# Kernel tuning notes

Hardware: AMD Instinct MI355X
Metric: run time of the kernel (lower is better)

## Reference

```python
import jax, jax.numpy as jnp
import numpy as np

B, C, H, W = 2, 256, 120, 240
HID = 512  # mlp_ratio=2 * embed_dim
EPS = 1e-5


def setup_inputs() -> dict:
    key = jax.random.key(0)
    ks = jax.random.split(key, 10)
    f = lambda k, shp, s=1.0: jax.random.normal(k, shp, jnp.float32) * s
    return {
        'x': f(ks[0], (B, C, H, W)),
        'gamma': f(ks[1], (C,), 0.1),
        'beta': f(ks[2], (C,), 0.1),
        'norm0_w': jnp.ones((C,), jnp.float32),
        'norm0_b': jnp.zeros((C,), jnp.float32),
        'norm1_w': jnp.ones((C,), jnp.float32),
        'norm1_b': jnp.zeros((C,), jnp.float32),
        'w_spec_r': f(ks[3], (C, C), 0.02),
        'w_spec_i': f(ks[4], (C, C), 0.02),
        'inner_w': f(ks[5], (C, C), 0.02),
        'inner_b': jnp.zeros((C,), jnp.float32),
        'mlp_w1': f(ks[6], (HID, C), 0.02),
        'mlp_b1': jnp.zeros((HID,), jnp.float32),
        'mlp_w2': f(ks[7], (C, HID), 0.02),
        'mlp_b2': jnp.zeros((C,), jnp.float32),
    }


def _inorm(x, w, b):
    # InstanceNorm2d (affine): normalize over spatial dims per (batch, channel)
    m = x.mean(axis=(2, 3), keepdims=True)
    v = x.var(axis=(2, 3), keepdims=True)
    xh = (x - m) * jax.lax.rsqrt(v + EPS)
    return xh * w[None, :, None, None] + b[None, :, None, None]


def _conv1x1(x, w, b=None):
    y = jnp.einsum('bihw,oi->bohw', x, w)
    return y if b is None else y + b[None, :, None, None]


def reference(x, gamma, beta, norm0_w, norm0_b, norm1_w, norm1_b,
              w_spec_r, w_spec_i, inner_w, inner_b,
              mlp_w1, mlp_b1, mlp_w2, mlp_b2):
    residual = x
    h = _inorm(x, norm0_w, norm0_b)
    # SpectralConv2d: rfft2 -> channel-mixing complex matmul (all modes kept,
    # hard_thresholding_fraction=1.0) -> irfft2. sparsity_threshold=0 -> no shrink.
    xf = jnp.fft.rfft2(h, norm='ortho')                     # [B,C,H,W//2+1] complex
    wc = (w_spec_r + 1j * w_spec_i).astype(xf.dtype)
    yf = jnp.einsum('bihw,io->bohw', xf, wc)
    h = jnp.fft.irfft2(yf, s=(H, W), norm='ortho')
    # inner skip (1x1 conv of residual) + GELU (linear filter branch)
    h = h + _conv1x1(residual, inner_w, inner_b)
    h = jax.nn.gelu(h, approximate=False)
    h = _inorm(h, norm1_w, norm1_b)
    # FiLM with scale=1
    h = (1.0 + gamma[None, :, None, None]) * h + beta[None, :, None, None]
    # distributed MLP: 1x1 conv -> GELU -> 1x1 conv
    h = _conv1x1(h, mlp_w1, mlp_b1)
    h = jax.nn.gelu(h, approximate=False)
    h = _conv1x1(h, mlp_w2, mlp_b2)
    # outer skip = identity
    return h + residual
```

## Files before the change

### kernel.cpp

```cpp
#include <hip/hip_runtime.h>
#include <hip/hip_bf16.h>

typedef __hip_bfloat16 bf16;
typedef short short8 __attribute__((ext_vector_type(8)));
typedef float f32x4 __attribute__((ext_vector_type(4)));

#define NB 2
#define NC 256
#define NH 120
#define NW 240
#define NHW (NH*NW)
#define NSP 16384
#define NHID 512
#define NPT 450
#define REPS 1e-5f
#define SC_W 0.06454972243679028f
#define SC_H 0.09128709291752769f
#define PI2 6.283185307179586f

__device__ __forceinline__ float gelu_f(float x){ return 0.5f*x*(1.f+erff(x*0.7071067811865476f)); }
__device__ __forceinline__ float us2f(ushort u){ union{float f; uint v;} c; c.v=((uint)u)<<16; return c.f; }
__device__ __forceinline__ ushort f2us(float f){ bf16 b=__float2bfloat16(f); return *(ushort*)&b; }

#define OFF_A0   0
#define OFF_D0   512
#define OFF_A1c  1024
#define OFF_D1c  1536
#define OFF_TWF  2048
#define OFF_THF  34816
#define OFF_THI  67584
#define OFF_TWI  100352
#define OFF_WRT  133120
#define OFF_WIT  165888
#define OFF_IWB  198656
#define OFF_W2B  231424
#define OFF_W1P  296960
#define OFF_B1P  428032
#define OFF_PS   429056
#define OFF_RA   889856
#define OFF_RB   9278464
#define WS_FLOATS 17667072ULL

#define RA0 OFF_RA
#define RA1 (OFF_RA+4194304)
#define RB0 OFF_RB
#define RB1 (OFF_RB+4194304)
#define OFF_FRE RB0
#define OFF_FIM (RB0+3932160)

__global__ __launch_bounds__(256) void k_setup(float* ws, const float* wsr, const float* wsi,
                                               const float* iw, const float* w2){
  int t = blockIdx.x*256 + threadIdx.x;
  if (t < 65536){
    int n=t>>8, w=t&255; float v=0.f;
    if(w<NW){
      if(n<121){ v = cosf(PI2*(float)((n*w)%NW)/(float)NW)*SC_W; }
      else if(n>=128 && n<249){ int k=n-128; v = -sinf(PI2*(float)((k*w)%NW)/(float)NW)*SC_W; }
    }
    ((ushort*)(ws+OFF_TWF))[t]=f2us(v); return;
  } t-=65536;
  if (t < 65536){
    int n=t>>8, j=t&255; float v=0.f;
    int h = j&127; bool im = (j>=128);
    if(h<NH){
      if(n<128){ int m=n; if(m<NH){ float sn,cs; sincosf(PI2*(float)((m*h)%NH)/(float)NH,&sn,&cs);
        v = (im? sn : cs)*SC_H; } }
      else { int m=n-128; if(m<NH){ float sn,cs; sincosf(PI2*(float)((m*h)%NH)/(float)NH,&sn,&cs);
        v = (im? cs : -sn)*SC_H; } }
    }
    ((ushort*)(ws+OFF_THF))[t]=f2us(v); return;
  } t-=65536;
  if (t < 65536){
    int n=t>>8, j=t&255; float v=0.f;
    int m = j&127; bool im = (j>=128);
    if(m<NH){
      if(n<128){ int h=n; if(h<NH){ float sn,cs; sincosf(PI2*(float)((h*m)%NH)/(float)NH,&sn,&cs);
        v = (im? -sn : cs)*SC_H; } }
      else { int h=n-128; if(h<NH){ float sn,cs; sincosf(PI2*(float)((h*m)%NH)/(float)NH,&sn,&cs);
        v = (im? cs : sn)*SC_H; } }
    }
    ((ushort*)(ws+OFF_THI))[t]=f2us(v); return;
  } t-=65536;
  if (t < 65536){
    int w=t>>8, j=t&255; float v=0.f;
    if(w<NW){
      int k = j&127; bool im = (j>=128);
      if(k<121){
        float ck = (k==0||k==120)? 1.f : 2.f;
        float sn,cs; sincosf(PI2*(float)((w*k)%NW)/(float)NW,&sn,&cs);
        v = ck*(im? -sn : cs)*SC_W;
      }
    }
    ((ushort*)(ws+OFF_TWI))[t]=f2us(v); return;
  } t-=65536;
  if (t < 65536){ int o=t>>8,i=t&255; ((ushort*)(ws+OFF_WRT))[t]=f2us(wsr[i*NC+o]); return; } t-=65536;
  if (t < 65536){ int o=t>>8,i=t&255; ((ushort*)(ws+OFF_WIT))[t]=f2us(wsi[i*NC+o]); return; } t-=65536;
  if (t < 65536){ ((ushort*)(ws+OFF_IWB))[t]=f2us(iw[t]); return; } t-=65536;
  if (t < 131072){ ((ushort*)(ws+OFF_W2B))[t]=f2us(w2[t]); return; }
}

__global__ __launch_bounds__(256) void k_stats0(const float* x, const float* n0w, const float* n0b, float* ws){
  int g = blockIdx.x, c = g & (NC-1);
  const float4* xp = (const float4*)(x + (size_t)g*NHW);
  float s=0.f, q=0.f;
  for(int i=threadIdx.x;i<NHW/4;i+=256){
    float4 v=xp[i];
    s+=v.x+v.y+v.z+v.w;
    q=fmaf(v.x,v.x,fmaf(v.y,v.y,fmaf(v.z,v.z,fmaf(v.w,v.w,q))));
  }
  __shared__ float ls[4], lq[4];
  #pragma unroll
  for(int o=32;o>0;o>>=1){ s+=__shfl_down(s,o,64); q+=__shfl_down(q,o,64); }
  int lane=threadIdx.x&63, wid=threadIdx.x>>6;
  if(!lane){ ls[wid]=s; lq[wid]=q; }
  __syncthreads();
  if(!threadIdx.x){
    s=ls[0]+ls[1]+ls[2]+ls[3]; q=lq[0]+lq[1]+lq[2]+lq[3];
    float m=s*(1.f/NHW), var=q*(1.f/NHW)-m*m;
    float r=rsqrtf(var+REPS);
    float a=r*n0w[c];
    ws[OFF_A0+g]=a; ws[OFF_D0+g]=fmaf(-m,a,n0b[c]);
  }
}

__global__ __launch_bounds__(256) void k_norm(const float* x, float* ws){
  int h = blockIdx.x, g = blockIdx.y, t = threadIdx.x;
  float a = ws[OFF_A0+g], d = ws[OFF_D0+g];
  ushort v = 0;
  if(t < NW) v = f2us(fmaf(a, x[(size_t)g*NHW + (size_t)h*NW + t], d));
  ((ushort*)(ws+RA0))[(size_t)g*30720 + (size_t)h*256 + t] = v;
}

template<int SPLIT, int EPI>
__global__ __launch_bounds__(256) void k_sgemm(const ushort* Ap0, const ushort* Ap1, const ushort* Bm,
                                               ushort* O0, ushort* O1, ushort* Ub){
  int nb = blockIdx.x*64, mb = blockIdx.y*256;
  int tid = threadIdx.x, w = tid>>6, l = tid&63, lq = l>>4, lr = l&15;
  const ushort* ar0[4]; const ushort* ar1[4]; const ushort* br[4];
  #pragma unroll
  for(int mt=0;mt<4;mt++){
    size_t r = mb + w*64 + mt*16 + lr;
    ar0[mt] = Ap0 + r*(SPLIT?128:256) + lq*8;
    ar1[mt] = SPLIT ? (Ap1 + r*128 + lq*8) : ar0[mt];
  }
  #pragma unroll
  for(int nt=0;nt<4;nt++) br[nt] = Bm + (size_t)(nb + nt*16 + lr)*256 + lq*8;
  f32x4 acc[4][4] = {};
  #pragma unroll
  for(int kk=0;kk<8;kk++){
    int k = kk*32;
    short8 af[4], bfr[4];
    #pragma unroll
    for(int mt=0;mt<4;mt++){
      const ushort* p = SPLIT ? ((k<128 ? ar0[mt] : ar1[mt]) + (k&127)) : (ar0[mt] + k);
      af[mt] = *(const short8*)p;
    }
    #pragma unroll
    for(int nt=0;nt<4;nt++) bfr[nt] = *(const short8*)(br[nt]+k);
    #pragma unroll
    for(int mt=0;mt<4;mt++)
      #pragma unroll
      for(int nt=0;nt<4;nt++)
        acc[mt][nt] = __builtin_amdgcn_mfma_f32_16x16x32_bf16(af[mt], bfr[nt], acc[mt][nt], 0,0,0);
  }
  #pragma unroll
  for(int mt=0;mt<4;mt++){
    #pragma unroll
    for(int r=0;r<4;r++){
      int m = mb + w*64 + mt*16 + lq*4 + r;
      #pragma unroll
      for(int nt=0;nt<4;nt++){
        int n = nb + nt*16 + lr;
        float v = acc[mt][nt][r];
        if (EPI==0){
          if(n<128) O0[(size_t)m*128+n] = f2us(v);
          else      O1[(size_t)m*128+n-128] = f2us(v);
        } else {
          int g = m>>7, h = m&127;
          if(h<NH && n<NW) Ub[(size_t)g*NHW + (size_t)h*NW + n] = f2us(v);
        }
      }
    }
  }
}

__global__ __launch_bounds__(256) void k_t64(const ushort* src, ushort* dst, int srows, int sgstr){
  __shared__ ushort lt[64][72];
  int g=blockIdx.z, i0=blockIdx.y*64, p0=blockIdx.x*64;
  int t=threadIdx.x, r=t>>2, q=t&3;
  int row = i0 + r;
  uint4 u0=make_uint4(0,0,0,0), u1=u0;
  if(row < srows){
    const ushort* sp = src + (size_t)g*sgstr + (size_t)row*128 + p0 + q*16;
    u0=*(const uint4*)sp; u1=*(const uint4*)(sp+8);
  }
  *(uint4*)&lt[r][q*16]=u0; *(uint4*)&lt[r][q*16+8]=u1;
  __syncthreads();
  int pr=t>>2, q2=t&3;
  union { ushort s[8]; uint4 u; } o0, o1;
  #pragma unroll
  for(int e=0;e<8;e++){ o0.s[e]=lt[q2*16+e][pr]; o1.s[e]=lt[q2*16+8+e][pr]; }
  ushort* dp = dst + (size_t)g*NSP + (size_t)(p0+pr)*128 + i0 + q2*16;
  *(uint4*)dp = o0.u; *(uint4*)(dp+8) = o1.u;
}

__global__ __launch_bounds__(256) void k_tP(const ushort* src, ushort* dst){
  __shared__ ushort lt[64][72];
  int b=blockIdx.z, i0=blockIdx.y*64, p0=blockIdx.x*64;
  int t=threadIdx.x, r=t>>2, q=t&3;
  const ushort* sp = src + (size_t)(b*NC+i0+r)*NSP + p0 + q*16;
  uint4 u0=*(const uint4*)sp, u1=*(const uint4*)(sp+8);
  *(uint4*)&lt[r][q*16]=u0; *(uint4*)&lt[r][q*16+8]=u1;
  __syncthreads();
  int pr=t>>2, q2=t&3;
  union { ushort s[8]; uint4 u; } o0, o1;
  #pragma unroll
  for(int e=0;e<8;e++){ o0.s[e]=lt[q2*16+e][pr]; o1.s[e]=lt[q2*16+8+e][pr]; }
  ushort* dp = dst + ((size_t)b*NSP + p0 + pr)*NC + i0 + q2*16;
  *(uint4*)dp = o0.u; *(uint4*)(dp+8) = o1.u;
}

__global__ __launch_bounds__(256) void k_mixg(float* ws){
  int b = blockIdx.z, p0 = blockIdx.x*32;
  int tid = threadIdx.x, w = tid>>6, l = tid&63, lq = l>>4, lr = l&15;
  const ushort* Wr = (const ushort*)(ws+OFF_WRT);
  const ushort* Wi = (const ushort*)(ws+OFF_WIT);
  const ushort* Gr = (const ushort*)(ws+RA0) + (size_t)b*NSP*NC;
  const ushort* Gi = (const ushort*)(ws+RA1) + (size_t)b*NSP*NC;
  const ushort *wrr[4], *wir[4], *brr[2], *bir[2];
  #pragma unroll
  for(int mt=0;mt<4;mt++){ size_t ro=(size_t)(w*64+mt*16+lr)*NC+lq*8; wrr[mt]=Wr+ro; wir[mt]=Wi+ro; }
  #pragma unroll
  for(int nt=0;nt<2;nt++){ size_t ro=(size_t)(p0+nt*16+lr)*NC+lq*8; brr[nt]=Gr+ro; bir[nt]=Gi+ro; }
  f32x4 aR[4][2]={}, aI[4][2]={};
  for(int k=0;k<256;k+=32){
    short8 fr[4], fi[4], fin[4], gr[2], gi[2];
    #pragma unroll
    for(int mt=0;mt<4;mt++){
      fr[mt]=*(const short8*)(wrr[mt]+k);
      fi[mt]=*(const short8*)(wir[mt]+k);
      union { short8 s; uint u[4]; } nv; nv.s=fi[mt];
      nv.u[0]^=0x80008000u; nv.u[1]^=0x80008000u; nv.u[2]^=0x80008000u; nv.u[3]^=0x80008000u;
      fin[mt]=nv.s;
    }
    #pragma unroll
    for(int nt=0;nt<2;nt++){ gr[nt]=*(const short8*)(brr[nt]+k); gi[nt]=*(const short8*)(bir[nt]+k); }
    #pragma unroll
    for(int mt=0;mt<4;mt++)
      #pragma unroll
      for(int nt=0;nt<2;nt++){
        aR[mt][nt]=__builtin_amdgcn_mfma_f32_16x16x32_bf16(fr[mt], gr[nt], aR[mt][nt],0,0,0);
        aR[mt][nt]=__builtin_amdgcn_mfma_f32_16x16x32_bf16(fin[mt],gi[nt], aR[mt][nt],0,0,0);
        aI[mt][nt]=__builtin_amdgcn_mfma_f32_16x16x32_bf16(fi[mt], gr[nt], aI[mt][nt],0,0,0);
        aI[mt][nt]=__builtin_amdgcn_mfma_f32_16x16x32_bf16(fr[mt], gi[nt], aI[mt][nt],0,0,0);
      }
  }
  ushort* Yre = (ushort*)(ws+RB0);
  ushort* Yim = (ushort*)(ws+RB1);
  #pragma unroll
  for(int mt=0;mt<4;mt++){
    #pragma unroll
    for(int r=0;r<4;r++){
      int m = w*64 + mt*16 + lq*4 + r;
      #pragma unroll
      for(int nt=0;nt<2;nt++){
        int n = p0 + nt*16 + lr;
        size_t ad = (size_t)(b*NC+m)*NSP + n;
        Yre[ad] = f2us(aR[mt][nt][r]);
        Yim[ad] = f2us(aI[mt][nt][r]);
      }
    }
  }
}

__global__ __launch_bounds__(256,2) void k_inner(float* ws, const float* x, const float* ib){
  __shared__ ushort xt[64][264];
  int b = blockIdx.z, blk = blockIdx.x, p0 = blk*64;
  int t = threadIdx.x, w = t>>6, l = t&63, lq = l>>4, lr = l&15;
  #pragma unroll 4
  for(int cc=0; cc<16; cc++){
    int c = cc*16 + (t>>4);
    int p4 = (t&15)*4;
    float4 v = *(const float4*)(x + ((size_t)(b*NC+c))*NHW + p0 + p4);
    xt[p4  ][c]=f2us(v.x); xt[p4+1][c]=f2us(v.y);
    xt[p4+2][c]=f2us(v.z); xt[p4+3][c]=f2us(v.w);
  }
  __syncthreads();
  const ushort* W = (const ushort*)(ws+OFF_IWB);
  const ushort* ar[4];
  #pragma unroll
  for(int mt=0;mt<4;mt++) ar[mt] = W + (size_t)(w*64+mt*16+lr)*256 + lq*8;
  f32x4 acc[4][4] = {};
  #pragma unroll
  for(int kk=0;kk<8;kk++){
    int k = kk*32;
    short8 af[4], bfr[4];
    #pragma unroll
    for(int mt=0;mt<4;mt++) af[mt] = *(const short8*)(ar[mt]+k);
    #pragma unroll
    for(int nt=0;nt<4;nt++) bfr[nt] = *(const short8*)&xt[nt*16+lr][k+lq*8];
    #pragma unroll
    for(int mt=0;mt<4;mt++)
      #pragma unroll
      for(int nt=0;nt<4;nt++)
        acc[mt][nt] = __builtin_amdgcn_mfma_f32_16x16x32_bf16(af[mt], bfr[nt], acc[mt][nt], 0,0,0);
  }
  __syncthreads();
  const ushort* Usp = (const ushort*)(ws+OFF_RA);
  float* PS = ws + OFF_PS + ((size_t)(b*NPT+blk))*512;
  #pragma unroll
  for(int mt=0;mt<4;mt++){
    #pragma unroll
    for(int r=0;r<4;r++){
      int m = w*64 + mt*16 + lq*4 + r;
      float bb = ib[m];
      float ss = 0.f, sq = 0.f;
      #pragma unroll
      for(int nt=0;nt<4;nt++){
        int n = p0 + nt*16 + lr;
        float uv = us2f(Usp[((size_t)(b*NC+m))*NHW + n]);
        float g = gelu_f(acc[mt][nt][r] + bb + uv);
        xt[nt*16+lr][m] = f2us(g);
        ss += g; sq = fmaf(g,g,sq);
      }
      #pragma unroll
      for(int ofs=1; ofs<16; ofs<<=1){ ss += __shfl_xor(ss, ofs, 64); sq += __shfl_xor(sq, ofs, 64); }
      if(lr==0){ PS[m] = ss; PS[256+m] = sq; }
    }
  }
  __syncthreads();
  ushort* Up = (ushort*)(ws+OFF_RB);
  #pragma unroll
  for(int pp=0; pp<4; pp++){
    int p = pp*16 + (t>>4);
    int c0 = (t&15)*16;
    uint4 w0 = *(uint4*)&xt[p][c0];
    uint4 w1v = *(uint4*)&xt[p][c0+8];
    ushort* dp = Up + ((size_t)(b*NHW + p0 + p))*256 + c0;
    *(uint4*)dp = w0; *(uint4*)(dp+8) = w1v;
  }
}

__global__ __launch_bounds__(256) void k_stats1p(const float* gamma, const float* beta,
                                                 const float* n1w, const float* n1b, float* ws){
  int g = blockIdx.x, b = g>>8, c = g&255;
  float s=0.f, q=0.f;
  for(int i=threadIdx.x;i<NPT;i+=256){
    const float* P = ws + OFF_PS + ((size_t)(b*NPT+i))*512;
    s += P[c]; q += P[256+c];
  }
  __shared__ float ls[4], lq2[4];
  #pragma unroll
  for(int o=32;o>0;o>>=1){ s+=__shfl_down(s,o,64); q+=__shfl_down(q,o,64); }
  int lane=threadIdx.x&63, wid=threadIdx.x>>6;
  if(!lane){ ls[wid]=s; lq2[wid]=q; }
  __syncthreads();
  if(!threadIdx.x){
    s=ls[0]+ls[1]+ls[2]+ls[3]; q=lq2[0]+lq2[1]+lq2[2]+lq2[3];
    float m=s*(1.f/NHW), var=q*(1.f/NHW)-m*m;
    float r=rsqrtf(var+REPS);
    float gp1 = 1.f + gamma[c];
    float wv = n1w[c];
    ws[OFF_A1c+g] = gp1*wv*r;
    ws[OFF_D1c+g] = gp1*(n1b[c] - m*r*wv) + beta[c];
  }
}

__global__ __launch_bounds__(64) void k_fold(float* ws, const float* w1, const float* b1){
  int o = blockIdx.x, b = blockIdx.y, t = threadIdx.x;
  float acc = 0.f;
  ushort* W1p = (ushort*)(ws+OFF_W1P);
  #pragma unroll
  for(int ii=0; ii<4; ii++){
    int i = ii*64 + t;
    float wv = w1[o*256+i];
    W1p[((size_t)(b*NHID+o))*256 + i] = f2us(wv * ws[OFF_A1c + b*NC + i]);
    acc = fmaf(wv, ws[OFF_D1c + b*NC + i], acc);
  }
  #pragma unroll
  for(int ofs=32; ofs; ofs>>=1) acc += __shfl_down(acc, ofs, 64);
  if(!t) ws[OFF_B1P + b*NHID + o] = acc + b1[o];
}

__global__ __launch_bounds__(256,2) void k_mlp(float* ws, const float* x, const float* b2, float* out){
  __shared__ ushort midT[64][520];
  int b = blockIdx.z, p0 = blockIdx.x*64;
  int t = threadIdx.x, w = t>>6, l = t&63, lq = l>>4, lr = l&15;
  const ushort* W1p = (const ushort*)(ws+OFF_W1P) + (size_t)b*NHID*256;
  const ushort* Up  = (const ushort*)(ws+OFF_RB);
  const ushort* ar[8]; const ushort* br[4];
  #pragma unroll
  for(int mt=0;mt<8;mt++) ar[mt] = W1p + (size_t)(w*128+mt*16+lr)*256 + lq*8;
  #pragma unroll
  for(int nt=0;nt<4;nt++) br[nt] = Up + ((size_t)(b*NHW + p0 + nt*16+lr))*256 + lq*8;
  f32x4 acc1[8][4] = {};
  #pragma unroll
  for(int kk=0;kk<8;kk++){
    int k = kk*32;
    short8 bfr[4];
    #pragma unroll
    for(int nt=0;nt<4;nt++) bfr[nt] = *(const short8*)(br[nt]+k);
    #pragma unroll
    for(int mt=0;mt<8;mt++){
      short8 af = *(const short8*)(ar[mt]+k);
      #pragma unroll
      for(int nt=0;nt<4;nt++)
        acc1[mt][nt] = __builtin_amdgcn_mfma_f32_16x16x32_bf16(af, bfr[nt], acc1[mt][nt], 0,0,0);
    }
  }
  const float* b1p = ws + OFF_B1P + b*NHID;
  #pragma unroll
  for(int mt=0;mt<8;mt++){
    #pragma unroll
    for(int r=0;r<4;r++){
      int m1 = w*128 + mt*16 + lq*4 + r;
      float bb = b1p[m1];
      #pragma unroll
      for(int nt=0;nt<4;nt++){
        int p = nt*16 + lr;
        midT[p][m1] = f2us(gelu_f(acc1[mt][nt][r] + bb));
      }
    }
  }
  __syncthreads();
  const ushort* W2 = (const ushort*)(ws+OFF_W2B);
  const ushort* a2[4];
  #pragma unroll
  for(int mt=0;mt<4;mt++) a2[mt] = W2 + (size_t)(w*64+mt*16+lr)*512 + lq*8;
  f32x4 acc2[4][4] = {};
  #pragma unroll
  for(int kk=0;kk<16;kk++){
    int k = kk*32;
    short8 af[4], bfr[4];
    #pragma unroll
    for(int mt=0;mt<4;mt++) af[mt] = *(const short8*)(a2[mt]+k);
    #pragma unroll
    for(int nt=0;nt<4;nt++) bfr[nt] = *(const short8*)&midT[nt*16+lr][k+lq*8];
    #pragma unroll
    for(int mt=0;mt<4;mt++)
      #pragma unroll
      for(int nt=0;nt<4;nt++)
        acc2[mt][nt] = __builtin_amdgcn_mfma_f32_16x16x32_bf16(af[mt], bfr[nt], acc2[mt][nt], 0,0,0);
  }
  #pragma unroll
  for(int mt=0;mt<4;mt++){
    #pragma unroll
    for(int r=0;r<4;r++){
      int om = w*64 + mt*16 + lq*4 + r;
      float bb = b2[om];
      #pragma unroll
      for(int nt=0;nt<4;nt++){
        int n = p0 + nt*16 + lr;
        size_t ad = ((size_t)(b*NC+om))*NHW + n;
        out[ad] = acc2[mt][nt][r] + bb + x[ad];
      }
    }
  }
}

extern "C" void kernel_launch(void* const* d_in, const int* in_sizes, int n_in,
                              void* d_out, int out_size, void* d_ws, size_t ws_size,
                              hipStream_t stream) {
  const float* x     = (const float*)d_in[0];
  const float* gamma = (const float*)d_in[1];
  const float* beta  = (const float*)d_in[2];
  const float* n0w   = (const float*)d_in[3];
  const float* n0b   = (const float*)d_in[4];
  const float* n1w   = (const float*)d_in[5];
  const float* n1b   = (const float*)d_in[6];
  const float* wsr   = (const float*)d_in[7];
  const float* wsi   = (const float*)d_in[8];
  const float* iw    = (const float*)d_in[9];
  const float* ib    = (const float*)d_in[10];
  const float* w1    = (const float*)d_in[11];
  const float* b1    = (const float*)d_in[12];
  const float* w2    = (const float*)d_in[13];
  const float* b2    = (const float*)d_in[14];
  float* ws = (float*)d_ws;
  float* out = (float*)d_out;
  if (ws_size < WS_FLOATS*4ULL) return;

  k_setup <<<dim3(2304), dim3(256), 0, stream>>>(ws, wsr, wsi, iw, w2);
  k_stats0<<<dim3(512),  dim3(256), 0, stream>>>(x, n0w, n0b, ws);
  k_norm  <<<dim3(120,512), dim3(256), 0, stream>>>(x, ws);
  k_sgemm<0,0><<<dim3(4,240), dim3(256), 0, stream>>>((const ushort*)(ws+RA0), (const ushort*)(ws+RA0),
      (const ushort*)(ws+OFF_TWF), (ushort*)(ws+OFF_FRE), (ushort*)(ws+OFF_FIM), nullptr);
  k_t64 <<<dim3(2,2,512), dim3(256), 0, stream>>>((const ushort*)(ws+OFF_FRE), (ushort*)(ws+RA0), NH, NH*128);
  k_t64 <<<dim3(2,2,512), dim3(256), 0, stream>>>((const ushort*)(ws+OFF_FIM), (ushort*)(ws+RA1), NH, NH*128);
  k_sgemm<1,0><<<dim3(4,256), dim3(256), 0, stream>>>((const ushort*)(ws+RA0), (const ushort*)(ws+RA1),
      (const ushort*)(ws+OFF_THF), (ushort*)(ws+RB0), (ushort*)(ws+RB1), nullptr);
  k_tP <<<dim3(256,4,2), dim3(256), 0, stream>>>((const ushort*)(ws+RB0), (ushort*)(ws+RA0));
  k_tP <<<dim3(256,4,2), dim3(256), 0, stream>>>((const ushort*)(ws+RB1), (ushort*)(ws+RA1));
  k_mixg <<<dim3(512,1,2), dim3(256), 0, stream>>>(ws);
  k_sgemm<1,0><<<dim3(4,256), dim3(256), 0, stream>>>((const ushort*)(ws+RB0), (const ushort*)(ws+RB1),
      (const ushort*)(ws+OFF_THI), (ushort*)(ws+RA0), (ushort*)(ws+RA1), nullptr);
  k_t64 <<<dim3(2,2,512), dim3(256), 0, stream>>>((const ushort*)(ws+RA0), (ushort*)(ws+RB0), 128, NSP);
  k_t64 <<<dim3(2,2,512), dim3(256), 0, stream>>>((const ushort*)(ws+RA1), (ushort*)(ws+RB1), 128, NSP);
  k_sgemm<1,1><<<dim3(4,256), dim3(256), 0, stream>>>((const ushort*)(ws+RB0), (const ushort*)(ws+RB1),
      (const ushort*)(ws+OFF_TWI), nullptr, nullptr, (ushort*)(ws+RA0));
  k_inner <<<dim3(NPT,1,2), dim3(256), 0, stream>>>(ws, x, ib);
  k_stats1p<<<dim3(512), dim3(256), 0, stream>>>(gamma, beta, n1w, n1b, ws);
  k_fold  <<<dim3(512,2), dim3(64), 0, stream>>>(ws, w1, b1);
  k_mlp   <<<dim3(NPT,1,2), dim3(256), 0, stream>>>(ws, x, b2, out);
}
```

Before: 649.5 us.

## Merge paired transpose launches and widen inner/MLP blocks with LDS staging

The paired transpose kernels for the real and imaginary parts are merged into single launches that pick their source and destination from blockIdx.z. k_inner now processes 128 pixels per 512-thread block. k_mlp now uses 512 threads: it stages the activation tile in LDS instead of reading it from global memory per wave, and splits the second GEMM's columns across wave halves. The goal is fewer launches, more waves per block for latency hiding, and less redundant global traffic, at the cost of larger LDS use per block and so possibly lower occupancy.

```diff
diff --git a/kernel.cpp b/kernel.cpp
--- a/kernel.cpp
+++ b/kernel.cpp
@@ -12,7 +12,6 @@
 #define NHW (NH*NW)
 #define NSP 16384
 #define NHID 512
-#define NPT 450
 #define REPS 1e-5f
 #define SC_W 0.06454972243679028f
 #define SC_H 0.09128709291752769f
@@ -184,9 +183,13 @@
   }
 }
 
-__global__ __launch_bounds__(256) void k_t64(const ushort* src, ushort* dst, int srows, int sgstr){
+__global__ __launch_bounds__(256) void k_t64d(const ushort* s0, ushort* d0, const ushort* s1, ushort* d1,
+                                              int srows, int sgstr){
   __shared__ ushort lt[64][72];
-  int g=blockIdx.z, i0=blockIdx.y*64, p0=blockIdx.x*64;
+  int z = blockIdx.z, g = z & 511;
+  const ushort* src = (z>=512)? s1 : s0;
+  ushort* dst = (z>=512)? d1 : d0;
+  int i0=blockIdx.y*64, p0=blockIdx.x*64;
   int t=threadIdx.x, r=t>>2, q=t&3;
   int row = i0 + r;
   uint4 u0=make_uint4(0,0,0,0), u1=u0;
@@ -204,9 +207,12 @@
   *(uint4*)dp = o0.u; *(uint4*)(dp+8) = o1.u;
 }
 
-__global__ __launch_bounds__(256) void k_tP(const ushort* src, ushort* dst){
+__global__ __launch_bounds__(256) void k_tPd(const ushort* s0, ushort* d0, const ushort* s1, ushort* d1){
   __shared__ ushort lt[64][72];
-  int b=blockIdx.z, i0=blockIdx.y*64, p0=blockIdx.x*64;
+  int z=blockIdx.z, b=z&1;
+  const ushort* src = (z>=2)? s1 : s0;
+  ushort* dst = (z>=2)? d1 : d0;
+  int i0=blockIdx.y*64, p0=blockIdx.x*64;
   int t=threadIdx.x, r=t>>2, q=t&3;
   const ushort* sp = src + (size_t)(b*NC+i0+r)*NSP + p0 + q*16;
   uint4 u0=*(const uint4*)sp, u1=*(const uint4*)(sp+8);
@@ -273,23 +279,24 @@
   }
 }
 
-__global__ __launch_bounds__(256,2) void k_inner(float* ws, const float* x, const float* ib){
-  __shared__ ushort xt[64][264];
-  int b = blockIdx.z, blk = blockIdx.x, p0 = blk*64;
+__global__ __launch_bounds__(512,4) void k_inner(float* ws, const float* x, const float* ib){
+  __shared__ ushort xt[128*264];
+  int b = blockIdx.z, blk = blockIdx.x, p0 = blk*128;
   int t = threadIdx.x, w = t>>6, l = t&63, lq = l>>4, lr = l&15;
   #pragma unroll 4
   for(int cc=0; cc<16; cc++){
-    int c = cc*16 + (t>>4);
-    int p4 = (t&15)*4;
+    int c = cc*16 + (t>>5);
+    int p4 = (t&31)*4;
     float4 v = *(const float4*)(x + ((size_t)(b*NC+c))*NHW + p0 + p4);
-    xt[p4  ][c]=f2us(v.x); xt[p4+1][c]=f2us(v.y);
-    xt[p4+2][c]=f2us(v.z); xt[p4+3][c]=f2us(v.w);
+    xt[(p4  )*264+c]=f2us(v.x); xt[(p4+1)*264+c]=f2us(v.y);
+    xt[(p4+2)*264+c]=f2us(v.z); xt[(p4+3)*264+c]=f2us(v.w);
   }
   __syncthreads();
   const ushort* W = (const ushort*)(ws+OFF_IWB);
+  int mw = w&3, ph = (w>>2)*64;
   const ushort* ar[4];
   #pragma unroll
-  for(int mt=0;mt<4;mt++) ar[mt] = W + (size_t)(w*64+mt*16+lr)*256 + lq*8;
+  for(int mt=0;mt<4;mt++) ar[mt] = W + (size_t)(mw*64+mt*16+lr)*256 + lq*8;
   f32x4 acc[4][4] = {};
   #pragma unroll
   for(int kk=0;kk<8;kk++){
@@ -298,7 +305,7 @@
     #pragma unroll
     for(int mt=0;mt<4;mt++) af[mt] = *(const short8*)(ar[mt]+k);
     #pragma unroll
-    for(int nt=0;nt<4;nt++) bfr[nt] = *(const short8*)&xt[nt*16+lr][k+lq*8];
+    for(int nt=0;nt<4;nt++) bfr[nt] = *(const short8*)&xt[(ph+nt*16+lr)*264 + k + lq*8];
     #pragma unroll
     for(int mt=0;mt<4;mt++)
       #pragma unroll
@@ -307,20 +314,21 @@
   }
   __syncthreads();
   const ushort* Usp = (const ushort*)(ws+OFF_RA);
-  float* PS = ws + OFF_PS + ((size_t)(b*NPT+blk))*512;
+  float* PS = ws + OFF_PS + ((size_t)(b*450 + blk*2 + (w>>2)))*512;
   #pragma unroll
   for(int mt=0;mt<4;mt++){
     #pragma unroll
     for(int r=0;r<4;r++){
-      int m = w*64 + mt*16 + lq*4 + r;
+      int m = mw*64 + mt*16 + lq*4 + r;
       float bb = ib[m];
       float ss = 0.f, sq = 0.f;
       #pragma unroll
       for(int nt=0;nt<4;nt++){
-        int n = p0 + nt*16 + lr;
+        int pl = ph + nt*16 + lr;
+        int n = p0 + pl;
         float uv = us2f(Usp[((size_t)(b*NC+m))*NHW + n]);
         float g = gelu_f(acc[mt][nt][r] + bb + uv);
-        xt[nt*16+lr][m] = f2us(g);
+        xt[pl*264 + m] = f2us(g);
         ss += g; sq = fmaf(g,g,sq);
       }
       #pragma unroll
@@ -330,14 +338,12 @@
   }
   __syncthreads();
   ushort* Up = (ushort*)(ws+OFF_RB);
-  #pragma unroll
-  for(int pp=0; pp<4; pp++){
-    int p = pp*16 + (t>>4);
-    int c0 = (t&15)*16;
-    uint4 w0 = *(uint4*)&xt[p][c0];
-    uint4 w1v = *(uint4*)&xt[p][c0+8];
+  {
+    int p = t>>2, c0 = (t&3)*64;
+    const ushort* sp = &xt[p*264 + c0];
     ushort* dp = Up + ((size_t)(b*NHW + p0 + p))*256 + c0;
-    *(uint4*)dp = w0; *(uint4*)(dp+8) = w1v;
+    #pragma unroll
+    for(int e=0;e<8;e++) ((uint4*)dp)[e] = ((const uint4*)sp)[e];
   }
 }
 
@@ -345,8 +351,8 @@
                                                  const float* n1w, const float* n1b, float* ws){
   int g = blockIdx.x, b = g>>8, c = g&255;
   float s=0.f, q=0.f;
-  for(int i=threadIdx.x;i<NPT;i+=256){
-    const float* P = ws + OFF_PS + ((size_t)(b*NPT+i))*512;
+  for(int i=threadIdx.x;i<450;i+=256){
+    const float* P = ws + OFF_PS + ((size_t)(b*450+i))*512;
     s += P[c]; q += P[256+c];
   }
   __shared__ float ls[4], lq2[4];
@@ -382,75 +388,82 @@
   if(!t) ws[OFF_B1P + b*NHID + o] = acc + b1[o];
 }
 
-__global__ __launch_bounds__(256,2) void k_mlp(float* ws, const float* x, const float* b2, float* out){
-  __shared__ ushort midT[64][520];
+__global__ __launch_bounds__(512,4) void k_mlp(float* ws, const float* x, const float* b2, float* out){
+  __shared__ ushort lds[66560];
   int b = blockIdx.z, p0 = blockIdx.x*64;
   int t = threadIdx.x, w = t>>6, l = t&63, lq = l>>4, lr = l&15;
+  {
+    int p = t>>3, c0 = (t&7)*32;
+    const ushort* sp = (const ushort*)(ws+OFF_RB) + ((size_t)(b*NHW + p0 + p))*256 + c0;
+    uint4 v0=((const uint4*)sp)[0], v1=((const uint4*)sp)[1], v2=((const uint4*)sp)[2], v3=((const uint4*)sp)[3];
+    ushort* dp = &lds[p*264 + c0];
+    ((uint4*)dp)[0]=v0; ((uint4*)dp)[1]=v1; ((uint4*)dp)[2]=v2; ((uint4*)dp)[3]=v3;
+  }
+  __syncthreads();
   const ushort* W1p = (const ushort*)(ws+OFF_W1P) + (size_t)b*NHID*256;
-  const ushort* Up  = (const ushort*)(ws+OFF_RB);
-  const ushort* ar[8]; const ushort* br[4];
-  #pragma unroll
-  for(int mt=0;mt<8;mt++) ar[mt] = W1p + (size_t)(w*128+mt*16+lr)*256 + lq*8;
-  #pragma unroll
-  for(int nt=0;nt<4;nt++) br[nt] = Up + ((size_t)(b*NHW + p0 + nt*16+lr))*256 + lq*8;
-  f32x4 acc1[8][4] = {};
+  const ushort* ar[4];
+  #pragma unroll
+  for(int mt=0;mt<4;mt++) ar[mt] = W1p + (size_t)(w*64+mt*16+lr)*256 + lq*8;
+  f32x4 acc1[4][4] = {};
   #pragma unroll
   for(int kk=0;kk<8;kk++){
     int k = kk*32;
-    short8 bfr[4];
-    #pragma unroll
-    for(int nt=0;nt<4;nt++) bfr[nt] = *(const short8*)(br[nt]+k);
-    #pragma unroll
-    for(int mt=0;mt<8;mt++){
-      short8 af = *(const short8*)(ar[mt]+k);
+    short8 af[4], bfr[4];
+    #pragma unroll
+    for(int mt=0;mt<4;mt++) af[mt] = *(const short8*)(ar[mt]+k);
+    #pragma unroll
+    for(int nt=0;nt<4;nt++) bfr[nt] = *(const short8*)&lds[(nt*16+lr)*264 + k + lq*8];
+    #pragma unroll
+    for(int mt=0;mt<4;mt++)
       #pragma unroll
       for(int nt=0;nt<4;nt++)
-        acc1[mt][nt] = __builtin_amdgcn_mfma_f32_16x16x32_bf16(af, bfr[nt], acc1[mt][nt], 0,0,0);
-    }
-  }
+        acc1[mt][nt] = __builtin_amdgcn_mfma_f32_16x16x32_bf16(af[mt], bfr[nt], acc1[mt][nt], 0,0,0);
+  }
+  __syncthreads();
   const float* b1p = ws + OFF_B1P + b*NHID;
   #pragma unroll
-  for(int mt=0;mt<8;mt++){
+  for(int mt=0;mt<4;mt++){
     #pragma unroll
     for(int r=0;r<4;r++){
-      int m1 = w*128 + mt*16 + lq*4 + r;
+      int m1 = w*64 + mt*16 + lq*4 + r;
       float bb = b1p[m1];
       #pragma unroll
       for(int nt=0;nt<4;nt++){
         int p = nt*16 + lr;
-        midT[p][m1] = f2us(gelu_f(acc1[mt][nt][r] + bb));
+        lds[p*520 + m1] = f2us(gelu_f(acc1[mt][nt][r] + bb));
       }
     }
   }
   __syncthreads();
   const ushort* W2 = (const ushort*)(ws+OFF_W2B);
+  int mw = w&3, nh = (w>>2)*32;
   const ushort* a2[4];
   #pragma unroll
-  for(int mt=0;mt<4;mt++) a2[mt] = W2 + (size_t)(w*64+mt*16+lr)*512 + lq*8;
-  f32x4 acc2[4][4] = {};
+  for(int mt=0;mt<4;mt++) a2[mt] = W2 + (size_t)(mw*64+mt*16+lr)*512 + lq*8;
+  f32x4 acc2[4][2] = {};
   #pragma unroll
   for(int kk=0;kk<16;kk++){
     int k = kk*32;
-    short8 af[4], bfr[4];
+    short8 af[4], bfr[2];
     #pragma unroll
     for(int mt=0;mt<4;mt++) af[mt] = *(const short8*)(a2[mt]+k);
     #pragma unroll
-    for(int nt=0;nt<4;nt++) bfr[nt] = *(const short8*)&midT[nt*16+lr][k+lq*8];
+    for(int nt=0;nt<2;nt++) bfr[nt] = *(const short8*)&lds[(nh+nt*16+lr)*520 + k + lq*8];
     #pragma unroll
     for(int mt=0;mt<4;mt++)
       #pragma unroll
-      for(int nt=0;nt<4;nt++)
+      for(int nt=0;nt<2;nt++)
         acc2[mt][nt] = __builtin_amdgcn_mfma_f32_16x16x32_bf16(af[mt], bfr[nt], acc2[mt][nt], 0,0,0);
   }
   #pragma unroll
   for(int mt=0;mt<4;mt++){
     #pragma unroll
     for(int r=0;r<4;r++){
-      int om = w*64 + mt*16 + lq*4 + r;
+      int om = mw*64 + mt*16 + lq*4 + r;
       float bb = b2[om];
       #pragma unroll
-      for(int nt=0;nt<4;nt++){
-        int n = p0 + nt*16 + lr;
+      for(int nt=0;nt<2;nt++){
+        int n = p0 + nh + nt*16 + lr;
         size_t ad = ((size_t)(b*NC+om))*NHW + n;
         out[ad] = acc2[mt][nt][r] + bb + x[ad];
       }
@@ -485,21 +498,21 @@
   k_norm  <<<dim3(120,512), dim3(256), 0, stream>>>(x, ws);
   k_sgemm<0,0><<<dim3(4,240), dim3(256), 0, stream>>>((const ushort*)(ws+RA0), (const ushort*)(ws+RA0),
       (const ushort*)(ws+OFF_TWF), (ushort*)(ws+OFF_FRE), (ushort*)(ws+OFF_FIM), nullptr);
-  k_t64 <<<dim3(2,2,512), dim3(256), 0, stream>>>((const ushort*)(ws+OFF_FRE), (ushort*)(ws+RA0), NH, NH*128);
-  k_t64 <<<dim3(2,2,512), dim3(256), 0, stream>>>((const ushort*)(ws+OFF_FIM), (ushort*)(ws+RA1), NH, NH*128);
+  k_t64d <<<dim3(2,2,1024), dim3(256), 0, stream>>>((const ushort*)(ws+OFF_FRE), (ushort*)(ws+RA0),
+      (const ushort*)(ws+OFF_FIM), (ushort*)(ws+RA1), NH, NH*128);
   k_sgemm<1,0><<<dim3(4,256), dim3(256), 0, stream>>>((const ushort*)(ws+RA0), (const ushort*)(ws+RA1),
       (const ushort*)(ws+OFF_THF), (ushort*)(ws+RB0), (ushort*)(ws+RB1), nullptr);
-  k_tP <<<dim3(256,4,2), dim3(256), 0, stream>>>((const ushort*)(ws+RB0), (ushort*)(ws+RA0));
-  k_tP <<<dim3(256,4,2), dim3(256), 0, stream>>>((const ushort*)(ws+RB1), (ushort*)(ws+RA1));
+  k_tPd <<<dim3(256,4,4), dim3(256), 0, stream>>>((const ushort*)(ws+RB0), (ushort*)(ws+RA0),
+      (const ushort*)(ws+RB1), (ushort*)(ws+RA1));
   k_mixg <<<dim3(512,1,2), dim3(256), 0, stream>>>(ws);
   k_sgemm<1,0><<<dim3(4,256), dim3(256), 0, stream>>>((const ushort*)(ws+RB0), (const ushort*)(ws+RB1),
       (const ushort*)(ws+OFF_THI), (ushort*)(ws+RA0), (ushort*)(ws+RA1), nullptr);
-  k_t64 <<<dim3(2,2,512), dim3(256), 0, stream>>>((const ushort*)(ws+RA0), (ushort*)(ws+RB0), 128, NSP);
-  k_t64 <<<dim3(2,2,512), dim3(256), 0, stream>>>((const ushort*)(ws+RA1), (ushort*)(ws+RB1), 128, NSP);
+  k_t64d <<<dim3(2,2,1024), dim3(256), 0, stream>>>((const ushort*)(ws+RA0), (ushort*)(ws+RB0),
+      (const ushort*)(ws+RA1), (ushort*)(ws+RB1), 128, NSP);
   k_sgemm<1,1><<<dim3(4,256), dim3(256), 0, stream>>>((const ushort*)(ws+RB0), (const ushort*)(ws+RB1),
       (const ushort*)(ws+OFF_TWI), nullptr, nullptr, (ushort*)(ws+RA0));
-  k_inner <<<dim3(NPT,1,2), dim3(256), 0, stream>>>(ws, x, ib);
+  k_inner <<<dim3(225,1,2), dim3(512), 0, stream>>>(ws, x, ib);
   k_stats1p<<<dim3(512), dim3(256), 0, stream>>>(gamma, beta, n1w, n1b, ws);
   k_fold  <<<dim3(512,2), dim3(64), 0, stream>>>(ws, w1, b1);
-  k_mlp   <<<dim3(NPT,1,2), dim3(256), 0, stream>>>(ws, x, b2, out);
-}
+  k_mlp   <<<dim3(450,1,2), dim3(512), 0, stream>>>(ws, x, b2, out);
+}
```

Result: slower. 731.3 us (+12.6%).
